# Kernel optimization log

Measured on AMD Instinct MI355X. Metric: run time of the kernel, lower is better.

The kernel has to match this reference:

```python
import jax, jax.numpy as jnp
import numpy as np

B, G, D = 256, 64, 20          # batch, genes per term, subsystem output dim
T3, T2, T1, T0 = 2048, 512, 128, 1  # terms per stratum, deepest first
FAN = 4                        # children per internal term (root gets all T1)
EPS = 1e-5                     # BatchNorm1d eps


def setup_inputs() -> dict:
    key = jax.random.key(0)
    ks = jax.random.split(key, 32)
    def genes(k, T):
        # binary gene perturbation states (column 3 of go_gene_strata_state)
        return (jax.random.uniform(k, (B, T, G)) < 0.5).astype(jnp.float32)
    def lin(kw, kb, T, din):
        # nn.init.uniform_(w, -0.001, 0.001) per DCellSubsystem
        W = jax.random.uniform(kw, (T, din, D), minval=-0.001, maxval=0.001)
        b = jax.random.uniform(kb, (T, D), minval=-0.001, maxval=0.001)
        return W, b
    in3, in2, in1, in0 = G, FAN * D + G, FAN * D + G, T1 * D + G
    W3, b3 = lin(ks[0], ks[1], T3, in3)
    W2, b2 = lin(ks[2], ks[3], T2, in2)
    W1, b1 = lin(ks[4], ks[5], T1, in1)
    W0, b0 = lin(ks[6], ks[7], T0, in0)
    ones = lambda T: jnp.ones((T, D), jnp.float32)
    zeros = lambda T: jnp.zeros((T, D), jnp.float32)
    hw0 = jax.random.normal(ks[8], (T0, D, 1)) * 0.1
    hb0 = jnp.zeros((T0, 1), jnp.float32)
    return {
        'genes3': genes(ks[9], T3), 'genes2': genes(ks[10], T2),
        'genes1': genes(ks[11], T1), 'genes0': genes(ks[12], T0),
        'W3': W3, 'b3': b3, 'g3': ones(T3), 'be3': zeros(T3),
        'W2': W2, 'b2': b2, 'g2': ones(T2), 'be2': zeros(T2),
        'W1': W1, 'b1': b1, 'g1': ones(T1), 'be1': zeros(T1),
        'W0': W0, 'b0': b0, 'g0': ones(T0), 'be0': zeros(T0),
        'hw0': hw0, 'hb0': hb0,
    }


def _subsystem(x, W, b, g, be):
    # Linear -> BatchNorm1d (training mode, batch stats over axis 0) -> Tanh
    z = jnp.einsum('bti,tio->bto', x, W) + b          # [B, T, D]
    mu = jnp.mean(z, axis=0)
    var = jnp.var(z, axis=0)                           # biased, as in torch BN
    zn = (z - mu) * jax.lax.rsqrt(var + EPS)
    return jnp.tanh(zn * g + be)


def reference(genes3, genes2, genes1, genes0,
              W3, b3, g3, be3, W2, b2, g2, be2,
              W1, b1, g1, be1, W0, b0, g0, be0, hw0, hb0):
    # stratum 3 (leaves): input is gene states only
    h3 = _subsystem(genes3, W3, b3, g3, be3)           # [B, T3, D]
    # stratum 2: concat FAN contiguous children + own gene states
    x2 = jnp.concatenate([h3.reshape(B, T2, FAN * D), genes2], axis=-1)
    h2 = _subsystem(x2, W2, b2, g2, be2)               # [B, T2, D]
    x1 = jnp.concatenate([h2.reshape(B, T1, FAN * D), genes1], axis=-1)
    h1 = _subsystem(x1, W1, b1, g1, be1)               # [B, T1, D]
    # root: all T1 children + root gene states
    x0 = jnp.concatenate([h1.reshape(B, T0, T1 * D), genes0], axis=-1)
    h0 = _subsystem(x0, W0, b0, g0, be0)               # [B, 1, D]
    pred = jnp.einsum('bto,toc->btc', h0, hw0) + hb0   # root linear head
    return pred.reshape(B, 1)
```

## Files before the change

kernel.cpp:

```cpp
#include <hip/hip_runtime.h>
#include <hip/hip_fp16.h>


#define DEV static __device__ __forceinline__

constexpr int B_  = 256, G_ = 64, D_ = 20;
constexpr int T3_ = 2048, T2_ = 512, T1_ = 128;
constexpr float EPS_ = 1e-5f;

constexpr size_t OFF_GT3 = 0;
constexpr size_t SZ_GT3 = (size_t)T3_ * B_ * G_ * 2;
constexpr size_t OFF_GT2 = OFF_GT3 + SZ_GT3;
constexpr size_t SZ_GT2 = (size_t)T2_ * B_ * G_ * 2;
constexpr size_t OFF_GT1 = OFF_GT2 + SZ_GT2;
constexpr size_t SZ_GT1 = (size_t)T1_ * B_ * G_ * 2;
constexpr size_t OFF_H3B = OFF_GT1 + SZ_GT1;
constexpr size_t SZ_H3 = (size_t)T3_ * B_ * D_ * 2;
constexpr size_t OFF_H2B = OFF_H3B + SZ_H3;
constexpr size_t SZ_H2 = (size_t)T2_ * B_ * D_ * 2;
constexpr size_t OFF_H1B = OFF_H2B + SZ_H2;
constexpr size_t SZ_H1 = (size_t)B_ * T1_ * D_ * 4;
constexpr size_t OFF_Z0B = OFF_H1B + SZ_H1;

typedef _Float16 half8_t __attribute__((ext_vector_type(8)));
typedef float f32x4 __attribute__((ext_vector_type(4)));

DEV half8_t as_h8(uint4 u) {
    union { uint4 u4; half8_t h; } c; c.u4 = u; return c.h;
}

DEV float fast_tanh(float x) {
    float e = __expf(2.0f * x);
    return fmaf(-2.0f, __builtin_amdgcn_rcpf(e + 1.0f), 1.0f);
}

template <int T>
__global__ __launch_bounds__(256, 4) void k_transpose(const float* __restrict__ genes,
                                                      __half* __restrict__ gT) {
    __shared__ uint lds[64 * 4 * 33];
    const int b0 = (blockIdx.x & 3) * 64;
    const int t0 = (blockIdx.x >> 2) * 4;
    const int tid = threadIdx.x, w = tid >> 6, l = tid & 63;
#pragma unroll
    for (int i = 0; i < 16; ++i) {
        const int b_loc = w * 16 + i;
        float4 f = ((const float4*)(genes + ((size_t)(b0 + b_loc) * T + t0) * G_))[l];
        const int t = l >> 4, g4 = l & 15;
        union { __half2 h; uint u; } a, c;
        a.h = __floats2half2_rn(f.x, f.y);
        c.h = __floats2half2_rn(f.z, f.w);
        uint* row = lds + (b_loc * 4 + t) * 33;
        row[2 * g4]     = a.u;
        row[2 * g4 + 1] = c.u;
    }
    __syncthreads();
#pragma unroll
    for (int r = 0; r < 8; ++r) {
        const int M = tid + 256 * r;
        const int t = M >> 9, b = (M >> 3) & 63, u4 = M & 7;
        const uint* row = lds + (b * 4 + t) * 33 + 4 * u4;
        uint4 v = make_uint4(row[0], row[1], row[2], row[3]);
        ((uint4*)(gT + (((size_t)(t0 + t) * B_) + b0 + b) * G_))[u4] = v;
    }
}

template <int T, int NCHILD, bool OUT_HALF>
__global__ __launch_bounds__(256, 4) void k_gemm(const __half* __restrict__ hsrc,
                                                 const __half* __restrict__ gT,
                                                 const float* __restrict__ W,
                                                 const float* __restrict__ g,
                                                 const float* __restrict__ be,
                                                 void* __restrict__ hout_) {
    constexpr int K_IN = NCHILD * 20 + 64;
    constexpr int NK = NCHILD + 2;
    constexpr int STRB = NCHILD ? 200 : 72;
    __shared__ __half WT[32 * STRB];
    __shared__ float gv[D_], bev[D_];
    __shared__ float sred[4][16], qred[4][16];

    const int t = blockIdx.x, tid = threadIdx.x;

    uint* WTu = (uint*)WT;
    for (int j = tid; j < 32 * STRB / 2; j += 256) WTu[j] = 0;
    if (tid < D_) { gv[tid] = g[t * D_ + tid]; bev[tid] = be[t * D_ + tid]; }
    __syncthreads();
    const float* Wt = W + (size_t)t * (K_IN * D_);
    for (int j = tid; j < K_IN * D_; j += 256) {
        int k_orig = j / D_, o = j - k_orig * D_;
        int k_lds;
        if (NCHILD && k_orig < NCHILD * D_) {
            int c = k_orig / D_;
            k_lds = c * 32 + (k_orig - c * D_);
        } else {
            k_lds = NCHILD * 32 + (k_orig - NCHILD * D_);
        }
        WT[o * STRB + k_lds] = __float2half(Wt[j]);
    }
    __syncthreads();

    const int w = tid >> 6, lane = tid & 63;
    const int quad = lane >> 4, l15 = lane & 15;
    const int nt = w >> 1, mhalf = w & 1;
    const int ocol = nt * 16 + l15;
    const int brow_base = mhalf * 128;

    half8_t Bf[NK];
#pragma unroll
    for (int ks = 0; ks < NK; ++ks)
        Bf[ks] = as_h8(*(const uint4*)(WT + ocol * STRB + ks * 32 + quad * 8));

    f32x4 acc[8];
#pragma unroll
    for (int mt = 0; mt < 8; ++mt) acc[mt] = (f32x4){0.f, 0.f, 0.f, 0.f};

#pragma unroll
    for (int mt = 0; mt < 8; ++mt) {
        const int bA = brow_base + mt * 16 + l15;
#pragma unroll
        for (int c = 0; c < NCHILD; ++c) {
            const __half* ap = hsrc + ((size_t)(NCHILD * t + c) * B_ + bA) * D_ + quad * 8;
            uint2 u0 = *(const uint2*)(ap);
            uint2 u1 = *(const uint2*)(ap + 4);
            acc[mt] = __builtin_amdgcn_mfma_f32_16x16x32_f16(
                as_h8(make_uint4(u0.x, u0.y, u1.x, u1.y)), Bf[c], acc[mt], 0, 0, 0);
        }
        const __half* gp = gT + ((size_t)t * B_ + bA) * G_ + quad * 8;
#pragma unroll
        for (int ks = 0; ks < 2; ++ks) {
            uint4 au = *(const uint4*)(gp + ks * 32);
            acc[mt] = __builtin_amdgcn_mfma_f32_16x16x32_f16(
                as_h8(au), Bf[NCHILD + ks], acc[mt], 0, 0, 0);
        }
    }

    float s = 0.f, q = 0.f;
#pragma unroll
    for (int mt = 0; mt < 8; ++mt)
#pragma unroll
        for (int r = 0; r < 4; ++r) {
            float z = acc[mt][r];
            s += z; q += z * z;
        }
    s += __shfl_xor(s, 16, 64); q += __shfl_xor(q, 16, 64);
    s += __shfl_xor(s, 32, 64); q += __shfl_xor(q, 32, 64);
    if (lane < 16) { sred[w][lane] = s; qred[w][lane] = q; }
    __syncthreads();
    const float S = sred[2 * nt][l15] + sred[2 * nt + 1][l15];
    const float Q = qred[2 * nt][l15] + qred[2 * nt + 1][l15];
    const float mu  = S * (1.0f / B_);
    const float var = fmaxf(Q * (1.0f / B_) - mu * mu, 0.0f);
    const float rstd = rsqrtf(var + EPS_);
    const int oc = ocol < D_ ? ocol : D_ - 1;
    const float A = rstd * gv[oc];
    const float C = bev[oc] - mu * A;

    if (ocol < D_) {
#pragma unroll
        for (int mt = 0; mt < 8; ++mt)
#pragma unroll
            for (int r = 0; r < 4; ++r) {
                float h = fast_tanh(fmaf(A, acc[mt][r], C));
                int b = brow_base + mt * 16 + quad * 4 + r;
                if (OUT_HALF) {
                    ((__half*)hout_)[((size_t)t * B_ + b) * D_ + ocol] = __float2half(h);
                } else {
                    ((float*)hout_)[((size_t)b * T + t) * D_ + ocol] = h;
                }
            }
    }
}

__global__ __launch_bounds__(256, 4) void k_stage0a(const float* __restrict__ h1,
                                                    const float* __restrict__ genes0,
                                                    const float* __restrict__ W0,
                                                    float* __restrict__ z0p) {
    const int b = blockIdx.x >> 2, s = blockIdx.x & 3, tid = threadIdx.x;
    const int kbase = 640 * s;
    const float* x = h1 + (size_t)b * (T1_ * D_);
    float acc[D_] = {};
#pragma unroll
    for (int j = 0; j < 3; ++j) {
        int kl = tid + 256 * j;
        if (kl < 640) {
            int k = kbase + kl;
            float xk = x[k];
            const float4* w = (const float4*)(W0 + (size_t)k * D_);
#pragma unroll
            for (int v = 0; v < D_ / 4; ++v) {
                float4 f = w[v];
                acc[4 * v + 0] = fmaf(xk, f.x, acc[4 * v + 0]);
                acc[4 * v + 1] = fmaf(xk, f.y, acc[4 * v + 1]);
                acc[4 * v + 2] = fmaf(xk, f.z, acc[4 * v + 2]);
                acc[4 * v + 3] = fmaf(xk, f.w, acc[4 * v + 3]);
            }
        }
    }
    if (s == 3 && tid < G_) {
        float xk = genes0[(size_t)b * G_ + tid];
        const float4* w = (const float4*)(W0 + (size_t)(T1_ * D_ + tid) * D_);
#pragma unroll
        for (int v = 0; v < D_ / 4; ++v) {
            float4 f = w[v];
            acc[4 * v + 0] = fmaf(xk, f.x, acc[4 * v + 0]);
            acc[4 * v + 1] = fmaf(xk, f.y, acc[4 * v + 1]);
            acc[4 * v + 2] = fmaf(xk, f.z, acc[4 * v + 2]);
            acc[4 * v + 3] = fmaf(xk, f.w, acc[4 * v + 3]);
        }
    }
    __shared__ float sred[4][D_];
    const int lane = tid & 63, wave = tid >> 6;
#pragma unroll
    for (int off = 32; off; off >>= 1)
#pragma unroll
        for (int o = 0; o < D_; ++o) acc[o] += __shfl_xor(acc[o], off, 64);
    if (lane == 0)
#pragma unroll
        for (int o = 0; o < D_; ++o) sred[wave][o] = acc[o];
    __syncthreads();
    if (tid < D_)
        z0p[((size_t)b * 4 + s) * D_ + tid] =
            sred[0][tid] + sred[1][tid] + sred[2][tid] + sred[3][tid];
}

__global__ __launch_bounds__(256) void k_stage0b(const float* __restrict__ z0p,
                                                 const float* __restrict__ g0,
                                                 const float* __restrict__ be0,
                                                 const float* __restrict__ hw0,
                                                 const float* __restrict__ hb0,
                                                 float* __restrict__ out) {
    const int tid = threadIdx.x;
    float acc[D_] = {};
#pragma unroll
    for (int s = 0; s < 4; ++s) {
        const float4* zp = (const float4*)(z0p + ((size_t)tid * 4 + s) * D_);
#pragma unroll
        for (int v = 0; v < D_ / 4; ++v) {
            float4 f = zp[v];
            acc[4 * v + 0] += f.x; acc[4 * v + 1] += f.y;
            acc[4 * v + 2] += f.z; acc[4 * v + 3] += f.w;
        }
    }
    __shared__ float sred[4][D_], qred[4][D_], Avec[D_], Cvec[D_], hwv[D_ + 1];
    const int lane = tid & 63, wave = tid >> 6;
    float s[D_], q[D_];
#pragma unroll
    for (int o = 0; o < D_; ++o) { s[o] = acc[o]; q[o] = acc[o] * acc[o]; }
#pragma unroll
    for (int off = 32; off; off >>= 1) {
#pragma unroll
        for (int o = 0; o < D_; ++o) {
            s[o] += __shfl_xor(s[o], off, 64);
            q[o] += __shfl_xor(q[o], off, 64);
        }
    }
    if (lane == 0) {
#pragma unroll
        for (int o = 0; o < D_; ++o) { sred[wave][o] = s[o]; qred[wave][o] = q[o]; }
    }
    __syncthreads();
    if (tid < D_) {
        float S = sred[0][tid] + sred[1][tid] + sred[2][tid] + sred[3][tid];
        float Q = qred[0][tid] + qred[1][tid] + qred[2][tid] + qred[3][tid];
        float mu  = S * (1.0f / B_);
        float var = fmaxf(Q * (1.0f / B_) - mu * mu, 0.0f);
        float rstd = rsqrtf(var + EPS_);
        float A = rstd * g0[tid];
        Avec[tid] = A;
        Cvec[tid] = be0[tid] - mu * A;
        hwv[tid] = hw0[tid];
    }
    if (tid == 0) hwv[D_] = hb0[0];
    __syncthreads();
    float pred = hwv[D_];
#pragma unroll
    for (int o = 0; o < D_; ++o) {
        float h = fast_tanh(fmaf(acc[o], Avec[o], Cvec[o]));
        pred = fmaf(h, hwv[o], pred);
    }
    out[tid] = pred;
}

extern "C" void kernel_launch(void* const* d_in, const int* in_sizes, int n_in,
                              void* d_out, int out_size, void* d_ws, size_t ws_size,
                              hipStream_t stream) {
    const float* genes3 = (const float*)d_in[0];
    const float* genes2 = (const float*)d_in[1];
    const float* genes1 = (const float*)d_in[2];
    const float* genes0 = (const float*)d_in[3];
    const float* W3  = (const float*)d_in[4];
    const float* g3  = (const float*)d_in[6];
    const float* be3 = (const float*)d_in[7];
    const float* W2  = (const float*)d_in[8];
    const float* g2  = (const float*)d_in[10];
    const float* be2 = (const float*)d_in[11];
    const float* W1  = (const float*)d_in[12];
    const float* g1  = (const float*)d_in[14];
    const float* be1 = (const float*)d_in[15];
    const float* W0  = (const float*)d_in[16];
    const float* g0  = (const float*)d_in[18];
    const float* be0 = (const float*)d_in[19];
    const float* hw0 = (const float*)d_in[20];
    const float* hb0 = (const float*)d_in[21];

    char* wsb = (char*)d_ws;
    __half* gT3 = (__half*)(wsb + OFF_GT3);
    __half* gT2 = (__half*)(wsb + OFF_GT2);
    __half* gT1 = (__half*)(wsb + OFF_GT1);
    __half* h3  = (__half*)(wsb + OFF_H3B);
    __half* h2  = (__half*)(wsb + OFF_H2B);
    float*  h1  = (float*)(wsb + OFF_H1B);
    float*  z0p = (float*)(wsb + OFF_Z0B);

    k_transpose<T3_><<<T3_, 256, 0, stream>>>(genes3, gT3);
    k_transpose<T2_><<<T2_, 256, 0, stream>>>(genes2, gT2);
    k_transpose<T1_><<<T1_, 256, 0, stream>>>(genes1, gT1);

    k_gemm<T3_, 0, true ><<<T3_, 256, 0, stream>>>(nullptr, gT3, W3, g3, be3, h3);
    k_gemm<T2_, 4, true ><<<T2_, 256, 0, stream>>>(h3, gT2, W2, g2, be2, h2);
    k_gemm<T1_, 4, false><<<T1_, 256, 0, stream>>>(h2, gT1, W1, g1, be1, h1);
    k_stage0a<<<B_ * 4, 256, 0, stream>>>(h1, genes0, W0, z0p);
    k_stage0b<<<1, 256, 0, stream>>>(z0p, g0, be0, hw0, hb0, (float*)d_out);
}
```

Before: 366.9 us.

## Store transposed gene states as u8 and merge transpose kernels into one launch

The transposed gene-state buffers now hold one byte per gene instead of fp16, and the GEMM kernels expand each byte to 0/1 halves in registers by bit tricks before the MFMA. This halves the write traffic of the transpose and the read traffic of the gene operand in every stratum GEMM. The three per-stratum transpose launches are also merged into one grid that branches on block index. The byte conversion is exact only because the gene inputs are binary 0/1, so it relies on that property of the input data and would truncate any other values.

```diff
diff --git a/kernel.cpp b/kernel.cpp
--- a/kernel.cpp
+++ b/kernel.cpp
@@ -8,12 +8,14 @@
 constexpr int T3_ = 2048, T2_ = 512, T1_ = 128;
 constexpr float EPS_ = 1e-5f;
 
+typedef unsigned char u8;
+
 constexpr size_t OFF_GT3 = 0;
-constexpr size_t SZ_GT3 = (size_t)T3_ * B_ * G_ * 2;
+constexpr size_t SZ_GT3 = (size_t)T3_ * B_ * G_;
 constexpr size_t OFF_GT2 = OFF_GT3 + SZ_GT3;
-constexpr size_t SZ_GT2 = (size_t)T2_ * B_ * G_ * 2;
+constexpr size_t SZ_GT2 = (size_t)T2_ * B_ * G_;
 constexpr size_t OFF_GT1 = OFF_GT2 + SZ_GT2;
-constexpr size_t SZ_GT1 = (size_t)T1_ * B_ * G_ * 2;
+constexpr size_t SZ_GT1 = (size_t)T1_ * B_ * G_;
 constexpr size_t OFF_H3B = OFF_GT1 + SZ_GT1;
 constexpr size_t SZ_H3 = (size_t)T3_ * B_ * D_ * 2;
 constexpr size_t OFF_H2B = OFF_H3B + SZ_H3;
@@ -29,44 +31,58 @@
     union { uint4 u4; half8_t h; } c; c.u4 = u; return c.h;
 }
 
+DEV half8_t u8x8_to_h8(uint2 v) {
+    uint4 r;
+    uint x = v.x;
+    r.x = ((x & 0xFFu) | ((x & 0xFF00u) << 8)) * 0x3C00u;
+    r.y = (((x >> 16) & 0xFFu) | ((x >> 8) & 0xFF0000u)) * 0x3C00u;
+    x = v.y;
+    r.z = ((x & 0xFFu) | ((x & 0xFF00u) << 8)) * 0x3C00u;
+    r.w = (((x >> 16) & 0xFFu) | ((x >> 8) & 0xFF0000u)) * 0x3C00u;
+    return as_h8(r);
+}
+
 DEV float fast_tanh(float x) {
     float e = __expf(2.0f * x);
     return fmaf(-2.0f, __builtin_amdgcn_rcpf(e + 1.0f), 1.0f);
 }
 
-template <int T>
-__global__ __launch_bounds__(256, 4) void k_transpose(const float* __restrict__ genes,
-                                                      __half* __restrict__ gT) {
-    __shared__ uint lds[64 * 4 * 33];
-    const int b0 = (blockIdx.x & 3) * 64;
-    const int t0 = (blockIdx.x >> 2) * 4;
+__global__ __launch_bounds__(256, 4) void k_transpose_all(
+        const float* __restrict__ g3s, const float* __restrict__ g2s,
+        const float* __restrict__ g1s,
+        u8* __restrict__ d3, u8* __restrict__ d2, u8* __restrict__ d1) {
+    __shared__ uint lds[64 * 4 * 17];
+    int blk = blockIdx.x;
+    const float* src; u8* dst; int T;
+    if (blk < T3_)              { src = g3s; dst = d3; T = T3_; }
+    else if (blk < T3_ + T2_)   { blk -= T3_; src = g2s; dst = d2; T = T2_; }
+    else                        { blk -= T3_ + T2_; src = g1s; dst = d1; T = T1_; }
+    const int b0 = (blk & 3) * 64;
+    const int t0 = (blk >> 2) * 4;
     const int tid = threadIdx.x, w = tid >> 6, l = tid & 63;
 #pragma unroll
     for (int i = 0; i < 16; ++i) {
         const int b_loc = w * 16 + i;
-        float4 f = ((const float4*)(genes + ((size_t)(b0 + b_loc) * T + t0) * G_))[l];
+        float4 f = ((const float4*)(src + ((size_t)(b0 + b_loc) * T + t0) * G_))[l];
         const int t = l >> 4, g4 = l & 15;
-        union { __half2 h; uint u; } a, c;
-        a.h = __floats2half2_rn(f.x, f.y);
-        c.h = __floats2half2_rn(f.z, f.w);
-        uint* row = lds + (b_loc * 4 + t) * 33;
-        row[2 * g4]     = a.u;
-        row[2 * g4 + 1] = c.u;
-    }
-    __syncthreads();
-#pragma unroll
-    for (int r = 0; r < 8; ++r) {
+        uint p = (uint)(u8)f.x | ((uint)(u8)f.y << 8) |
+                 ((uint)(u8)f.z << 16) | ((uint)(u8)f.w << 24);
+        lds[(b_loc * 4 + t) * 17 + g4] = p;
+    }
+    __syncthreads();
+#pragma unroll
+    for (int r = 0; r < 4; ++r) {
         const int M = tid + 256 * r;
-        const int t = M >> 9, b = (M >> 3) & 63, u4 = M & 7;
-        const uint* row = lds + (b * 4 + t) * 33 + 4 * u4;
+        const int t = M >> 8, b = (M >> 2) & 63, c = M & 3;
+        const uint* row = lds + (b * 4 + t) * 17 + c * 4;
         uint4 v = make_uint4(row[0], row[1], row[2], row[3]);
-        ((uint4*)(gT + (((size_t)(t0 + t) * B_) + b0 + b) * G_))[u4] = v;
+        ((uint4*)(dst + (((size_t)(t0 + t) * B_) + b0 + b) * G_))[c] = v;
     }
 }
 
 template <int T, int NCHILD, bool OUT_HALF>
 __global__ __launch_bounds__(256, 4) void k_gemm(const __half* __restrict__ hsrc,
-                                                 const __half* __restrict__ gT,
+                                                 const u8* __restrict__ gT,
                                                  const float* __restrict__ W,
                                                  const float* __restrict__ g,
                                                  const float* __restrict__ be,
@@ -124,12 +140,12 @@
             acc[mt] = __builtin_amdgcn_mfma_f32_16x16x32_f16(
                 as_h8(make_uint4(u0.x, u0.y, u1.x, u1.y)), Bf[c], acc[mt], 0, 0, 0);
         }
-        const __half* gp = gT + ((size_t)t * B_ + bA) * G_ + quad * 8;
+        const u8* gp = gT + ((size_t)t * B_ + bA) * G_ + quad * 8;
 #pragma unroll
         for (int ks = 0; ks < 2; ++ks) {
-            uint4 au = *(const uint4*)(gp + ks * 32);
+            uint2 au = *(const uint2*)(gp + ks * 32);
             acc[mt] = __builtin_amdgcn_mfma_f32_16x16x32_f16(
-                as_h8(au), Bf[NCHILD + ks], acc[mt], 0, 0, 0);
+                u8x8_to_h8(au), Bf[NCHILD + ks], acc[mt], 0, 0, 0);
         }
     }
 
@@ -303,18 +319,16 @@
     const float* hb0 = (const float*)d_in[21];
 
     char* wsb = (char*)d_ws;
-    __half* gT3 = (__half*)(wsb + OFF_GT3);
-    __half* gT2 = (__half*)(wsb + OFF_GT2);
-    __half* gT1 = (__half*)(wsb + OFF_GT1);
+    u8* gT3 = (u8*)(wsb + OFF_GT3);
+    u8* gT2 = (u8*)(wsb + OFF_GT2);
+    u8* gT1 = (u8*)(wsb + OFF_GT1);
     __half* h3  = (__half*)(wsb + OFF_H3B);
     __half* h2  = (__half*)(wsb + OFF_H2B);
     float*  h1  = (float*)(wsb + OFF_H1B);
     float*  z0p = (float*)(wsb + OFF_Z0B);
 
-    k_transpose<T3_><<<T3_, 256, 0, stream>>>(genes3, gT3);
-    k_transpose<T2_><<<T2_, 256, 0, stream>>>(genes2, gT2);
-    k_transpose<T1_><<<T1_, 256, 0, stream>>>(genes1, gT1);
-
+    k_transpose_all<<<T3_ + T2_ + T1_, 256, 0, stream>>>(genes3, genes2, genes1,
+                                                         gT3, gT2, gT1);
     k_gemm<T3_, 0, true ><<<T3_, 256, 0, stream>>>(nullptr, gT3, W3, g3, be3, h3);
     k_gemm<T2_, 4, true ><<<T2_, 256, 0, stream>>>(h3, gT2, W2, g2, be2, h2);
     k_gemm<T1_, 4, false><<<T1_, 256, 0, stream>>>(h2, gT1, W1, g1, be1, h1);
```

Result: faster. 341.8 us (-6.8%).
